# Optimization experiments

Measured on AMD Instinct MI355X. Metric: run time of the kernel, lower is better.

## Reference

```python
import jax, jax.numpy as jnp
import numpy as np

BATCH = 32
IN_SHAPE = (64, 64)
OUT_SHAPE = (128, 128)


def setup_inputs() -> dict:
    key = jax.random.key(0)
    k1, k2 = jax.random.split(key)
    y = jax.random.normal(k1, (BATCH, *IN_SHAPE), dtype=jnp.float32)
    # normalized sample coordinates in [0,1), one per input dim
    xnew = jax.random.uniform(k2, (BATCH, *OUT_SHAPE, len(IN_SHAPE)), dtype=jnp.float32)
    return {"y": y, "xnew": xnew}


def reference(y, xnew):
    # y: [B, S1, S2]; xnew: [B, H, W, 2] with coords in [0,1)
    B = y.shape[0]
    s1, s2 = IN_SHAPE
    P = int(np.prod(OUT_SHAPE))
    x = xnew.reshape(B, P, 2)  # [B, P, 2]

    # FFT over spatial dims (dims 1..), as in torch.fft.fftn(..., dim=(1,2))
    F = jnp.fft.fftn(y, axes=(1, 2))  # [B, S1, S2] complex64

    # signed integer frequencies per dim (trigonometric interpolation)
    f1 = jnp.fft.fftfreq(s1).astype(jnp.float32) * s1  # [S1]
    f2 = jnp.fft.fftfreq(s2).astype(jnp.float32) * s2  # [S2]

    two_pi_i = 2j * jnp.pi
    # per-dim complex phase factors; separable NUFFT-type-2 evaluation
    E1 = jnp.exp(two_pi_i * x[..., 0:1] * f1)  # [B, P, S1]
    E2 = jnp.exp(two_pi_i * x[..., 1:2] * f2)  # [B, P, S2]

    # ynew[b,p] = (1/(S1*S2)) * sum_{k,m} F[b,k,m] E1[b,p,k] E2[b,p,m]
    ynew = jnp.einsum('bkm,bpk,bpm->bp', F, E1, E2) / (s1 * s2)
    ynew = jnp.real(ynew)
    return ynew.reshape(B, *OUT_SHAPE)
```

## Files before the change

### kernel.cpp

```cpp
#include <hip/hip_runtime.h>
#include <math.h>

#define PI_F  3.14159265358979323846f
#define C64_F 0.99879545620517239271f
#define S64_F 0.04906767432741801426f

typedef _Float16 f16x8 __attribute__((ext_vector_type(8)));
typedef float    f32x4 __attribute__((ext_vector_type(4)));


__global__ __launch_bounds__(256, 3)
void fourier_interp_mfma(const float* __restrict__ y,
                         const float* __restrict__ xnew,
                         float* __restrict__ out)
{
    __shared__ __align__(16) _Float16 Yth[64 * 72];
    __shared__ __align__(16) _Float16 Ytl[64 * 72];
    __shared__ float2 tab[64];
    __shared__ float4 S1[256];
    __shared__ float4 S2[256];
    __shared__ int    NS1[256], NS2[256];
    __shared__ float  Wpart[4];

    const int tid    = threadIdx.x;
    const int batch  = blockIdx.x >> 6;
    const int seg    = blockIdx.x & 63;
    const int gpbase = (batch << 14) + (seg << 8);

    float wsum = 0.0f;
    {
        const float4* srcY = (const float4*)(y + (batch << 12));
#pragma unroll
        for (int i = 0; i < 4; ++i) {
            const int f = tid + (i << 8);
            const float4 v = srcY[f];
            const int k = f >> 4;
            const int n = (f & 15) << 2;
            _Float16 h;
            h = (_Float16)v.x; Yth[(n+0)*72 + k] = h; Ytl[(n+0)*72 + k] = (_Float16)(v.x - (float)h);
            h = (_Float16)v.y; Yth[(n+1)*72 + k] = h; Ytl[(n+1)*72 + k] = (_Float16)(v.y - (float)h);
            h = (_Float16)v.z; Yth[(n+2)*72 + k] = h; Ytl[(n+2)*72 + k] = (_Float16)(v.z - (float)h);
            h = (_Float16)v.w; Yth[(n+3)*72 + k] = h; Ytl[(n+3)*72 + k] = (_Float16)(v.w - (float)h);
            const float sv = (v.x - v.y) + (v.z - v.w);
            wsum += (k & 1) ? -sv : sv;
        }
    }
#pragma unroll
    for (int off = 32; off > 0; off >>= 1)
        wsum += __shfl_down(wsum, off, 64);
    if ((tid & 63) == 0) Wpart[tid >> 6] = wsum;

    {
        const float2 xv = ((const float2*)xnew)[gpbase + tid];
        {
            const float x = xv.x;
            float sx, cx; sincosf(PI_F * x, &sx, &cx);
            const float g = x * 64.0f;
            const float j = rintf(g);
            const float fr = g - j;
            const int  ji = (int)j;
            const float sf = sinf(PI_F * fr);
            const float s64 = (ji & 1) ? -sf : sf;
            const float d = x - j * 0.015625f;
            const float cf = (fr == 0.0f) ? 64.0f
                                          : sf * cosf(PI_F * d) / sinf(PI_F * d);
            S1[tid]  = make_float4(sx, cx, s64, cf);
            NS1[tid] = ji & 63;
        }
        {
            const float x = xv.y;
            float sx, cx; sincosf(PI_F * x, &sx, &cx);
            const float g = x * 64.0f;
            const float j = rintf(g);
            const float fr = g - j;
            const int  ji = (int)j;
            const float sf = sinf(PI_F * fr);
            const float s64 = (ji & 1) ? -sf : sf;
            const float d = x - j * 0.015625f;
            const float cf = (fr == 0.0f) ? 64.0f
                                          : sf * cosf(PI_F * d) / sinf(PI_F * d);
            S2[tid]  = make_float4(sx, cx, s64, cf);
            NS2[tid] = ji & 63;
        }
    }
    if (tid < 64) {
        float sn, cn;
        sincosf(PI_F * (float)tid * (1.0f / 64.0f), &sn, &cn);
        tab[tid] = make_float2(cn, sn);
    }
    __syncthreads();

    const float W = (Wpart[0] + Wpart[1]) + (Wpart[2] + Wpart[3]);

    const int lane = tid & 63;
    const int wv   = tid >> 6;
    const int quad = lane >> 4;
    const int lrow = lane & 15;

#pragma unroll 1
    for (int mt = 0; mt < 4; ++mt) {
        const int mtbase = (wv << 6) + (mt << 4);
        const float4 s1 = S1[mtbase + lrow];
        const int n1fix = NS1[mtbase + lrow];

        f16x8 bh[2], bl[2];
#pragma unroll
        for (int kt = 0; kt < 2; ++kt) {
            const int n1b = (kt << 5) + (quad << 3);
            const float2 t0 = tab[n1b];
            float st = s1.x * t0.x - s1.y * t0.y;
            float ct = s1.y * t0.x + s1.x * t0.y;
#pragma unroll
            for (int j = 0; j < 8; ++j) {
                const float sgn = (j & 1) ? -s1.z : s1.z;
                float c = sgn * ct * __builtin_amdgcn_rcpf(st);
                c = (n1b + j == n1fix) ? s1.w : c;
                const _Float16 h = (_Float16)c;
                bh[kt][j] = h;
                bl[kt][j] = (_Float16)(c - (float)h);
                if (j < 7) {
                    const float st2 = st * C64_F - ct * S64_F;
                    ct = ct * C64_F + st * S64_F;
                    st = st2;
                }
            }
        }

        f32x4 acc[4];
#pragma unroll
        for (int nt = 0; nt < 4; ++nt) acc[nt] = (f32x4){0.f, 0.f, 0.f, 0.f};
#pragma unroll
        for (int nt = 0; nt < 4; ++nt) {
#pragma unroll
            for (int kt = 0; kt < 2; ++kt) {
                const int off = ((nt << 4) + lrow) * 72 + (kt << 5) + (quad << 3);
                const f16x8 ah = *(const f16x8*)&Yth[off];
                const f16x8 al = *(const f16x8*)&Ytl[off];
                acc[nt] = __builtin_amdgcn_mfma_f32_16x16x32_f16(ah, bh[kt], acc[nt], 0, 0, 0);
                acc[nt] = __builtin_amdgcn_mfma_f32_16x16x32_f16(ah, bl[kt], acc[nt], 0, 0, 0);
                acc[nt] = __builtin_amdgcn_mfma_f32_16x16x32_f16(al, bh[kt], acc[nt], 0, 0, 0);
            }
        }

        const float4 s2 = S2[mtbase + lrow];
        const int n2fix = NS2[mtbase + lrow];
        float red = 0.0f;
#pragma unroll
        for (int nt = 0; nt < 4; ++nt) {
#pragma unroll
            for (int reg = 0; reg < 4; ++reg) {
                const int n2 = (nt << 4) + (quad << 2) + reg;
                const float2 tb = tab[n2];
                const float st = s2.x * tb.x - s2.y * tb.y;
                const float ct = s2.y * tb.x + s2.x * tb.y;
                const float sgn = (reg & 1) ? -s2.z : s2.z;
                float c = sgn * ct * __builtin_amdgcn_rcpf(st);
                c = (n2 == n2fix) ? s2.w : c;
                red = fmaf(c, acc[nt][reg], red);
            }
        }
        red += __shfl_xor(red, 16, 64);
        red += __shfl_xor(red, 32, 64);
        if (lane < 16) {
            const float r = red - s1.z * s2.z * W;
            out[gpbase + mtbase + lane] = r * (1.0f / 4096.0f);
        }
    }
}

extern "C" void kernel_launch(void* const* d_in, const int* in_sizes, int n_in,
                              void* d_out, int out_size, void* d_ws, size_t ws_size,
                              hipStream_t stream)
{
    const float* y    = (const float*)d_in[0];
    const float* xnew = (const float*)d_in[1];
    float* out        = (float*)d_out;

    fourier_interp_mfma<<<2048, 256, 0, stream>>>(y, xnew, out);
}
```

Before: 90.17 us.

## Use hardware sin/cos, hoist A fragments into registers, recur twiddles

Replaces libm sincosf/sinf/cosf and division with the hardware v_sin/v_cos builtins and the rcp builtin in the setup phase. Loads the fp16 hi/lo Y fragments into registers once per wave instead of re-reading LDS in every mt iteration. Computes the second-dimension cotangent terms by angle-addition recurrence instead of a table load per element, and interleaves B-fragment generation with the MFMAs. This adds register pressure, and the hardware trig functions and recurrence may lose some accuracy.

```diff
diff --git a/kernel.cpp b/kernel.cpp
--- a/kernel.cpp
+++ b/kernel.cpp
@@ -7,6 +7,9 @@
 
 typedef _Float16 f16x8 __attribute__((ext_vector_type(8)));
 typedef float    f32x4 __attribute__((ext_vector_type(4)));
+
+__device__ __forceinline__ float sinpi_hw(float x) { return __builtin_amdgcn_sinf(0.5f * x); }
+__device__ __forceinline__ float cospi_hw(float x) { return __builtin_amdgcn_cosf(0.5f * x); }
 
 
 __global__ __launch_bounds__(256, 3)
@@ -54,40 +57,38 @@
         const float2 xv = ((const float2*)xnew)[gpbase + tid];
         {
             const float x = xv.x;
-            float sx, cx; sincosf(PI_F * x, &sx, &cx);
+            const float sx = sinpi_hw(x), cx = cospi_hw(x);
             const float g = x * 64.0f;
             const float j = rintf(g);
             const float fr = g - j;
             const int  ji = (int)j;
-            const float sf = sinf(PI_F * fr);
+            const float sf = sinpi_hw(fr);
             const float s64 = (ji & 1) ? -sf : sf;
             const float d = x - j * 0.015625f;
             const float cf = (fr == 0.0f) ? 64.0f
-                                          : sf * cosf(PI_F * d) / sinf(PI_F * d);
+                : sf * cospi_hw(d) * __builtin_amdgcn_rcpf(sinpi_hw(d));
             S1[tid]  = make_float4(sx, cx, s64, cf);
             NS1[tid] = ji & 63;
         }
         {
             const float x = xv.y;
-            float sx, cx; sincosf(PI_F * x, &sx, &cx);
+            const float sx = sinpi_hw(x), cx = cospi_hw(x);
             const float g = x * 64.0f;
             const float j = rintf(g);
             const float fr = g - j;
             const int  ji = (int)j;
-            const float sf = sinf(PI_F * fr);
+            const float sf = sinpi_hw(fr);
             const float s64 = (ji & 1) ? -sf : sf;
             const float d = x - j * 0.015625f;
             const float cf = (fr == 0.0f) ? 64.0f
-                                          : sf * cosf(PI_F * d) / sinf(PI_F * d);
+                : sf * cospi_hw(d) * __builtin_amdgcn_rcpf(sinpi_hw(d));
             S2[tid]  = make_float4(sx, cx, s64, cf);
             NS2[tid] = ji & 63;
         }
     }
-    if (tid < 64) {
-        float sn, cn;
-        sincosf(PI_F * (float)tid * (1.0f / 64.0f), &sn, &cn);
-        tab[tid] = make_float2(cn, sn);
-    }
+    if (tid < 64)
+        tab[tid] = make_float2(cospi_hw((float)tid * (1.0f / 64.0f)),
+                               sinpi_hw((float)tid * (1.0f / 64.0f)));
     __syncthreads();
 
     const float W = (Wpart[0] + Wpart[1]) + (Wpart[2] + Wpart[3]);
@@ -97,48 +98,52 @@
     const int quad = lane >> 4;
     const int lrow = lane & 15;
 
+    f16x8 Ah[4][2], Al[4][2];
+#pragma unroll
+    for (int nt = 0; nt < 4; ++nt)
+#pragma unroll
+        for (int kt = 0; kt < 2; ++kt) {
+            const int off = ((nt << 4) + lrow) * 72 + (kt << 5) + (quad << 3);
+            Ah[nt][kt] = *(const f16x8*)&Yth[off];
+            Al[nt][kt] = *(const f16x8*)&Ytl[off];
+        }
+
 #pragma unroll 1
     for (int mt = 0; mt < 4; ++mt) {
         const int mtbase = (wv << 6) + (mt << 4);
         const float4 s1 = S1[mtbase + lrow];
         const int n1fix = NS1[mtbase + lrow];
 
-        f16x8 bh[2], bl[2];
+        f32x4 acc[4];
+#pragma unroll
+        for (int nt = 0; nt < 4; ++nt) acc[nt] = (f32x4){0.f, 0.f, 0.f, 0.f};
+
 #pragma unroll
         for (int kt = 0; kt < 2; ++kt) {
             const int n1b = (kt << 5) + (quad << 3);
             const float2 t0 = tab[n1b];
             float st = s1.x * t0.x - s1.y * t0.y;
             float ct = s1.y * t0.x + s1.x * t0.y;
+            f16x8 bh, bl;
 #pragma unroll
             for (int j = 0; j < 8; ++j) {
                 const float sgn = (j & 1) ? -s1.z : s1.z;
                 float c = sgn * ct * __builtin_amdgcn_rcpf(st);
                 c = (n1b + j == n1fix) ? s1.w : c;
                 const _Float16 h = (_Float16)c;
-                bh[kt][j] = h;
-                bl[kt][j] = (_Float16)(c - (float)h);
+                bh[j] = h;
+                bl[j] = (_Float16)(c - (float)h);
                 if (j < 7) {
                     const float st2 = st * C64_F - ct * S64_F;
                     ct = ct * C64_F + st * S64_F;
                     st = st2;
                 }
             }
-        }
-
-        f32x4 acc[4];
 #pragma unroll
-        for (int nt = 0; nt < 4; ++nt) acc[nt] = (f32x4){0.f, 0.f, 0.f, 0.f};
-#pragma unroll
-        for (int nt = 0; nt < 4; ++nt) {
-#pragma unroll
-            for (int kt = 0; kt < 2; ++kt) {
-                const int off = ((nt << 4) + lrow) * 72 + (kt << 5) + (quad << 3);
-                const f16x8 ah = *(const f16x8*)&Yth[off];
-                const f16x8 al = *(const f16x8*)&Ytl[off];
-                acc[nt] = __builtin_amdgcn_mfma_f32_16x16x32_f16(ah, bh[kt], acc[nt], 0, 0, 0);
-                acc[nt] = __builtin_amdgcn_mfma_f32_16x16x32_f16(ah, bl[kt], acc[nt], 0, 0, 0);
-                acc[nt] = __builtin_amdgcn_mfma_f32_16x16x32_f16(al, bh[kt], acc[nt], 0, 0, 0);
+            for (int nt = 0; nt < 4; ++nt) {
+                acc[nt] = __builtin_amdgcn_mfma_f32_16x16x32_f16(Ah[nt][kt], bh, acc[nt], 0, 0, 0);
+                acc[nt] = __builtin_amdgcn_mfma_f32_16x16x32_f16(Ah[nt][kt], bl, acc[nt], 0, 0, 0);
+                acc[nt] = __builtin_amdgcn_mfma_f32_16x16x32_f16(Al[nt][kt], bh, acc[nt], 0, 0, 0);
             }
         }
 
@@ -147,16 +152,21 @@
         float red = 0.0f;
 #pragma unroll
         for (int nt = 0; nt < 4; ++nt) {
+            const int n2b = (nt << 4) + (quad << 2);
+            const float2 tb = tab[n2b];
+            float st = s2.x * tb.x - s2.y * tb.y;
+            float ct = s2.y * tb.x + s2.x * tb.y;
 #pragma unroll
             for (int reg = 0; reg < 4; ++reg) {
-                const int n2 = (nt << 4) + (quad << 2) + reg;
-                const float2 tb = tab[n2];
-                const float st = s2.x * tb.x - s2.y * tb.y;
-                const float ct = s2.y * tb.x + s2.x * tb.y;
                 const float sgn = (reg & 1) ? -s2.z : s2.z;
                 float c = sgn * ct * __builtin_amdgcn_rcpf(st);
-                c = (n2 == n2fix) ? s2.w : c;
+                c = (n2b + reg == n2fix) ? s2.w : c;
                 red = fmaf(c, acc[nt][reg], red);
+                if (reg < 3) {
+                    const float st2 = st * C64_F - ct * S64_F;
+                    ct = ct * C64_F + st * S64_F;
+                    st = st2;
+                }
             }
         }
         red += __shfl_xor(red, 16, 64);
```

New measurement: 86.97 us. 1.04x faster.
